# Optimization experiments

Hardware: AMD Instinct MI355X
Metric: run time of the kernel (lower is better)

Reference implementation:

```python
import jax, jax.numpy as jnp
import numpy as np

# static config (matches init_kwargs / input_specs)
LENS = (2048, 1024, 512, 256)   # per-level temporal lengths, sum = 3840
N, LQ, D_MODEL = 8, 2048, 256
M, L, P = 8, 4, 4               # heads, levels, points
D_HEAD = D_MODEL // M           # 32


def setup_inputs() -> dict:
    key = jax.random.key(0)
    ks = jax.random.split(key, 8)
    s = 0.02  # xavier-ish scale for 256-wide linears
    return {
        "query": jax.random.normal(ks[0], (N, LQ, D_MODEL), jnp.float32),
        "reference_points": jax.random.uniform(ks[1], (N, LQ, L, 1), dtype=jnp.float32),
        "input_flatten": jax.random.normal(ks[2], (N, sum(LENS), D_MODEL), jnp.float32),
        "input_temporal_lens": jnp.array(LENS, jnp.int32),
        "input_level_start_index": jnp.array(np.concatenate([[0], np.cumsum(LENS)[:-1]]), jnp.int32),
        "W_val": jax.random.normal(ks[3], (D_MODEL, D_MODEL), jnp.float32) * s,
        "b_val": jnp.zeros((D_MODEL,), jnp.float32),
        "W_off": jax.random.normal(ks[4], (M * L * P, D_MODEL), jnp.float32) * s,
        "b_off": jax.random.normal(ks[5], (M * L * P,), jnp.float32),  # mimics linspace bias init
        "W_attn": jax.random.normal(ks[6], (M * L * P, D_MODEL), jnp.float32) * s,
        "b_attn": jnp.zeros((M * L * P,), jnp.float32),
    }


def _sample_level(v, x, T):
    """1D bilinear sampling with zero padding, matching F.grid_sample
    (mode='bilinear', padding_mode='zeros', align_corners=False) on a (1,T) map.
    v: (N, T, M, D) level values; x: (N, Lq, M, P) normalized locations in [0,1].
    Returns (N, Lq, M, P, D)."""
    n, lq, m, p = x.shape
    ix = x * T - 0.5
    ix0 = jnp.floor(ix)
    w1 = (ix - ix0)[..., None]            # (N,Lq,M,P,1)
    i0 = ix0.astype(jnp.int32)

    def gather(idx):
        valid = ((idx >= 0) & (idx < T)).astype(v.dtype)
        idxc = jnp.clip(idx, 0, T - 1)
        flat = idxc.transpose(0, 1, 3, 2).reshape(n, lq * p, m)       # (N, Lq*P, M)
        g = jnp.take_along_axis(v, flat[..., None], axis=1)           # (N, Lq*P, M, D)
        g = g * valid.transpose(0, 1, 3, 2).reshape(n, lq * p, m)[..., None]
        return g.reshape(n, lq, p, m, -1).transpose(0, 1, 3, 2, 4)    # (N,Lq,M,P,D)

    return gather(i0) * (1.0 - w1) + gather(i0 + 1) * w1


def _deform_core(value, lens, loc, attn):
    """value: (N, S, M, D); loc: (N,Lq,M,L,P,1); attn: (N,Lq,M,L,P) -> (N,Lq,M*D)"""
    out = 0.0
    start = 0
    for lid, T in enumerate(lens):
        v = value[:, start:start + T]
        start += T
        s = _sample_level(v, loc[:, :, :, lid, :, 0], T)              # (N,Lq,M,P,D)
        out = out + jnp.einsum('nqmpd,nqmp->nqmd', s, attn[:, :, :, lid])
    n, lq, m, d = out.shape
    return out.reshape(n, lq, m * d)


def reference(query, reference_points, input_flatten, input_temporal_lens,
              input_level_start_index, W_val, b_val, W_off, b_off, W_attn, b_attn):
    lens = LENS  # static per-level lengths (needed for static slicing)
    value = (input_flatten @ W_val.T + b_val).reshape(N, sum(lens), M, D_HEAD)
    offs = (query @ W_off.T + b_off).reshape(N, LQ, M, L, P, 1)
    attn = jax.nn.softmax((query @ W_attn.T + b_attn).reshape(N, LQ, M, L * P), axis=-1)
    attn = attn.reshape(N, LQ, M, L, P)
    # reference_points last dim == 1, offset_normalizer=None branch
    norm = jnp.asarray(lens, query.dtype)[None, None, None, :, None, None]
    loc = reference_points[:, :, None, :, None, :] + offs / norm      # (N,Lq,M,L,P,1)
    # fp32 path of the torch module returns the core output WITHOUT output_proj
    return _deform_core(value, lens, loc, attn)
```

## Files before the change

kernel.cpp:

```cpp
#include <hip/hip_runtime.h>
#include <cstddef>

namespace {

constexpr int NB    = 8;
constexpr int LQn   = 2048;
constexpr int DM    = 256;
constexpr int S_TOT = 3840;

typedef __attribute__((ext_vector_type(8))) short  short8;
typedef __attribute__((ext_vector_type(4))) float  f32x4;
typedef __attribute__((ext_vector_type(8))) _Float16 half8;
typedef __attribute__((ext_vector_type(4))) _Float16 half4;
typedef __attribute__((ext_vector_type(2))) _Float16 half2v;

__device__ inline unsigned short f2bf(float f) {
  union { float f; unsigned u; } v; v.f = f;
  const unsigned u = v.u;
  return (unsigned short)((u + 0x7FFFu + ((u >> 16) & 1u)) >> 16);
}

__global__ __launch_bounds__(256) void gemm_bf16_k(
    const float* __restrict__ A_val, const float* __restrict__ A_prj,
    const float* __restrict__ W_val, const float* __restrict__ b_val,
    const float* __restrict__ W_off, const float* __restrict__ b_off,
    const float* __restrict__ W_att, const float* __restrict__ b_att,
    _Float16* __restrict__ out_val, _Float16* __restrict__ out_prj)
{
  __shared__ short As[128 * 64];
  __shared__ short Bs[128 * 64];

  const int tid  = threadIdx.x;
  const int lane = tid & 63;
  const int wid  = tid >> 6;
  const int wm   = wid >> 1;
  const int wn   = wid & 1;

  const int id = blockIdx.x;
  const float *A, *W, *bias;
  _Float16* out;
  int r0, c0;
  if (id < 480) {
    const int rb = id >> 1, c = id & 1;
    A = A_val; out = out_val; r0 = rb * 128; c0 = c * 128;
    W = W_val + (size_t)c0 * DM; bias = b_val + c0;
  } else {
    const int j = id - 480, rb = j >> 1, c = j & 1;
    A = A_prj; out = out_prj; r0 = rb * 128; c0 = c * 128;
    W = c ? W_att : W_off; bias = c ? b_att : b_off;
  }

  f32x4 acc[4][4] = {};

  float bv[4];
  #pragma unroll
  for (int ni = 0; ni < 4; ++ni)
    bv[ni] = bias[wn * 64 + ni * 16 + (lane & 15)];

  f32x4 pa0[4], pa1[4], pw0[4], pw1[4];

  auto load_tiles = [&](int k0) {
    #pragma unroll
    for (int i = 0; i < 4; ++i) {
      const int ch  = tid + i * 256;
      const int row = ch >> 3;
      const int kg  = ch & 7;
      const size_t goff = (size_t)(r0 + row) * DM + k0 + kg * 8;
      pa0[i] = *reinterpret_cast<const f32x4*>(&A[goff]);
      pa1[i] = *reinterpret_cast<const f32x4*>(&A[goff + 4]);
      const size_t woff = (size_t)row * DM + k0 + kg * 8;
      pw0[i] = *reinterpret_cast<const f32x4*>(&W[woff]);
      pw1[i] = *reinterpret_cast<const f32x4*>(&W[woff + 4]);
    }
  };

  load_tiles(0);

  for (int k = 0; k < 4; ++k) {
    #pragma unroll
    for (int i = 0; i < 4; ++i) {
      const int ch  = tid + i * 256;
      const int row = ch >> 3;
      const int kg  = ch & 7;
      short8 sa, sw;
      #pragma unroll
      for (int j = 0; j < 4; ++j) {
        sa[j]     = (short)f2bf(pa0[i][j]);
        sa[j + 4] = (short)f2bf(pa1[i][j]);
        sw[j]     = (short)f2bf(pw0[i][j]);
        sw[j + 4] = (short)f2bf(pw1[i][j]);
      }
      const int byte = row * 128 + ((kg * 16) ^ ((row & 7) << 4));
      *reinterpret_cast<short8*>(reinterpret_cast<char*>(As) + byte) = sa;
      *reinterpret_cast<short8*>(reinterpret_cast<char*>(Bs) + byte) = sw;
    }
    if (k < 3) load_tiles((k + 1) * 64);

    asm volatile("s_waitcnt lgkmcnt(0)" ::: "memory");
    __builtin_amdgcn_sched_barrier(0);
    __builtin_amdgcn_s_barrier();
    __builtin_amdgcn_sched_barrier(0);

    #pragma unroll
    for (int ks = 0; ks < 2; ++ks) {
      const int kb = (ks * 32 + (lane >> 4) * 8) * 2;
      short8 af[4], bf[4];
      #pragma unroll
      for (int mi = 0; mi < 4; ++mi) {
        const int row = wm * 64 + mi * 16 + (lane & 15);
        const int byte = row * 128 + (kb ^ ((row & 7) << 4));
        af[mi] = *reinterpret_cast<const short8*>(
            reinterpret_cast<const char*>(As) + byte);
      }
      #pragma unroll
      for (int ni = 0; ni < 4; ++ni) {
        const int col = wn * 64 + ni * 16 + (lane & 15);
        const int byte = col * 128 + (kb ^ ((col & 7) << 4));
        bf[ni] = *reinterpret_cast<const short8*>(
            reinterpret_cast<const char*>(Bs) + byte);
      }
      #pragma unroll
      for (int mi = 0; mi < 4; ++mi)
        #pragma unroll
        for (int ni = 0; ni < 4; ++ni)
          acc[mi][ni] = __builtin_amdgcn_mfma_f32_16x16x32_bf16(
              af[mi], bf[ni], acc[mi][ni], 0, 0, 0);
    }

    asm volatile("s_waitcnt lgkmcnt(0)" ::: "memory");
    __builtin_amdgcn_sched_barrier(0);
    __builtin_amdgcn_s_barrier();
    __builtin_amdgcn_sched_barrier(0);
  }

  #pragma unroll
  for (int mi = 0; mi < 4; ++mi) {
    const int row = r0 + wm * 64 + mi * 16 + (lane >> 4) * 4;
    #pragma unroll
    for (int ni = 0; ni < 4; ++ni) {
      const int col = c0 + wn * 64 + ni * 16 + (lane & 15);
      #pragma unroll
      for (int j = 0; j < 4; ++j)
        out[(size_t)(row + j) * DM + col] = (_Float16)(acc[mi][ni][j] + bv[ni]);
    }
  }
}

__global__ __launch_bounds__(512) void sample_k(
    const _Float16* __restrict__ proj,
    const float* __restrict__ refp,
    const _Float16* __restrict__ value,
    float* __restrict__ out)
{
  __shared__ uint4 tap_s[8][136];

  const int d     = blockIdx.x;
  const int n     = d & 7;
  const int chunk = d >> 3;
  const int row0q = n * LQn + chunk * 8;
  const int t     = threadIdx.x;

  const int lens[4]   = {2048, 1024, 512, 256};
  const int starts[4] = {0, 2048, 3072, 3584};

  if (t < 256) {
    const int q   = t >> 5;
    const int m   = (t >> 2) & 7;
    const int sub = t & 3;
    const int j0  = m * 16 + sub * 4;
    const size_t prow = (size_t)(row0q + q) * DM;

    const half4 offv = *reinterpret_cast<const half4*>(&proj[prow + j0]);
    const half4 lgv  = *reinterpret_cast<const half4*>(&proj[prow + 128 + j0]);
    float lg[4], off[4];
    #pragma unroll
    for (int i = 0; i < 4; ++i) { lg[i] = (float)lgv[i]; off[i] = (float)offv[i]; }

    float mx = fmaxf(fmaxf(lg[0], lg[1]), fmaxf(lg[2], lg[3]));
    mx = fmaxf(mx, __shfl_xor(mx, 1));
    mx = fmaxf(mx, __shfl_xor(mx, 2));
    float e[4], s = 0.f;
    #pragma unroll
    for (int i = 0; i < 4; ++i) { e[i] = __expf(lg[i] - mx); s += e[i]; }
    s += __shfl_xor(s, 1);
    s += __shfl_xor(s, 2);
    const float inv = 1.f / s;

    const int   T  = lens[sub];
    const int   st = starts[sub];
    const float fT = (float)T;
    const float rf = refp[(size_t)(row0q + q) * 4 + sub];
    #pragma unroll
    for (int i = 0; i < 4; ++i) {
      const float a  = e[i] * inv;
      const float ix = fmaf(rf, fT, off[i] - 0.5f);
      const float fl = floorf(ix);
      const float w1 = ix - fl;
      const int   i0 = (int)fl;
      const int   i1 = i0 + 1;
      const float wa = (i0 >= 0 && i0 < T) ? a * (1.f - w1) : 0.f;
      const float wb = (i1 >= 0 && i1 < T) ? a * w1 : 0.f;
      const int   r0b = (st + min(max(i0, 0), T - 1)) * 512;
      const int   r1b = (st + min(max(i1, 0), T - 1)) * 512;
      union { half2v h; unsigned u; } pw;
      pw.h.x = (_Float16)wa; pw.h.y = (_Float16)wb;
      uint4 ent; ent.x = pw.u; ent.y = (unsigned)r0b; ent.z = (unsigned)r1b; ent.w = 0u;
      tap_s[q][m * 17 + sub * 4 + i] = ent;
    }
  }
  __syncthreads();

  const int q  = t >> 6;
  const int l  = t & 63;
  const int m  = l >> 3;
  const int dg = l & 3;
  const int th = (l >> 2) & 1;
  const char* vb = reinterpret_cast<const char*>(value) +
                   (size_t)n * S_TOT * 512 + m * 64 + dg * 16;

  float acc[8] = {};
  #pragma unroll
  for (int i = 0; i < 8; ++i) {
    const uint4 e = tap_s[q][m * 17 + th * 8 + i];
    union { unsigned u; half2v h; } pw; pw.u = e.x;
    const float wa = (float)pw.h.x;
    const float wb = (float)pw.h.y;
    const half8 v0 = *reinterpret_cast<const half8*>(vb + e.y);
    const half8 v1 = *reinterpret_cast<const half8*>(vb + e.z);
    #pragma unroll
    for (int j = 0; j < 8; ++j)
      acc[j] = fmaf(wa, (float)v0[j], fmaf(wb, (float)v1[j], acc[j]));
  }

  #pragma unroll
  for (int j = 0; j < 8; ++j) acc[j] += __shfl_xor(acc[j], 4);

  if (th == 0) {
    float* op = &out[(size_t)(row0q + q) * DM + m * 32 + dg * 8];
    f32x4 o0 = {acc[0], acc[1], acc[2], acc[3]};
    f32x4 o1 = {acc[4], acc[5], acc[6], acc[7]};
    *reinterpret_cast<f32x4*>(op)     = o0;
    *reinterpret_cast<f32x4*>(op + 4) = o1;
  }
}

}

extern "C" void kernel_launch(void* const* d_in, const int* in_sizes, int n_in,
                              void* d_out, int out_size, void* d_ws, size_t ws_size,
                              hipStream_t stream) {
  const float* query  = (const float*)d_in[0];
  const float* refp   = (const float*)d_in[1];
  const float* inflat = (const float*)d_in[2];
  const float* W_val  = (const float*)d_in[5];
  const float* b_val  = (const float*)d_in[6];
  const float* W_off  = (const float*)d_in[7];
  const float* b_off  = (const float*)d_in[8];
  const float* W_attn = (const float*)d_in[9];
  const float* b_attn = (const float*)d_in[10];
  float* out = (float*)d_out;

  _Float16* value_h = (_Float16*)d_ws;
  _Float16* proj_h  = (_Float16*)((char*)d_ws +
                      (size_t)NB * S_TOT * DM * sizeof(_Float16));

  gemm_bf16_k<<<dim3(736), dim3(256), 0, stream>>>(
      inflat, query, W_val, b_val, W_off, b_off, W_attn, b_attn,
      value_h, proj_h);

  sample_k<<<dim3(NB * LQn / 8), dim3(512), 0, stream>>>(
      proj_h, refp, value_h, out);
}
```

Before: 43.93 us.

## Pre-convert weights to swizzled bf16 blob and stream via global_load_lds

A small kernel now converts the three weight matrices once per call into a pre-swizzled bf16 blob. The GEMM then loads each B tile straight into LDS with global_load_lds, which drops the per-block fp32 weight loads, the bf16 conversion and the LDS stores. This cuts register pressure and weight bandwidth in the main GEMM, at the cost of an extra kernel launch and a finer vmcnt wait that is sensitive to the order of outstanding loads.

```diff
diff --git a/kernel.cpp b/kernel.cpp
--- a/kernel.cpp
+++ b/kernel.cpp
@@ -20,11 +20,45 @@
   return (unsigned short)((u + 0x7FFFu + ((u >> 16) & 1u)) >> 16);
 }
 
+__device__ inline void load_lds16(const void* g, void* l) {
+  __builtin_amdgcn_global_load_lds(
+      (const __attribute__((address_space(1))) void*)g,
+      (__attribute__((address_space(3))) void*)l, 16, 0, 0);
+}
+
+__global__ __launch_bounds__(256) void wconv_k(
+    const float* __restrict__ W_val, const float* __restrict__ W_off,
+    const float* __restrict__ W_att, unsigned short* __restrict__ blob)
+{
+  const int g     = blockIdx.x * 256 + threadIdx.x;
+  const int tile  = g >> 10;
+  const int ch    = g & 1023;
+  const int which = tile >> 2;
+  const int kt    = tile & 3;
+  const int row   = ch >> 3;
+  const int kg    = (ch & 7) ^ (row & 7);
+  const float* src;
+  if (which == 0)      src = W_val + (size_t)row * DM;
+  else if (which == 1) src = W_val + (size_t)(128 + row) * DM;
+  else if (which == 2) src = W_off + (size_t)row * DM;
+  else                 src = W_att + (size_t)row * DM;
+  const int col = kt * 64 + kg * 8;
+  const f32x4 w0 = *reinterpret_cast<const f32x4*>(&src[col]);
+  const f32x4 w1 = *reinterpret_cast<const f32x4*>(&src[col + 4]);
+  short8 s;
+  #pragma unroll
+  for (int j = 0; j < 4; ++j) {
+    s[j]     = (short)f2bf(w0[j]);
+    s[j + 4] = (short)f2bf(w1[j]);
+  }
+  *reinterpret_cast<short8*>(&blob[(size_t)g * 8]) = s;
+}
+
 __global__ __launch_bounds__(256) void gemm_bf16_k(
     const float* __restrict__ A_val, const float* __restrict__ A_prj,
-    const float* __restrict__ W_val, const float* __restrict__ b_val,
-    const float* __restrict__ W_off, const float* __restrict__ b_off,
-    const float* __restrict__ W_att, const float* __restrict__ b_att,
+    const unsigned short* __restrict__ wblob,
+    const float* __restrict__ b_val,
+    const float* __restrict__ b_off, const float* __restrict__ b_att,
     _Float16* __restrict__ out_val, _Float16* __restrict__ out_prj)
 {
   __shared__ short As[128 * 64];
@@ -37,18 +71,21 @@
   const int wn   = wid & 1;
 
   const int id = blockIdx.x;
-  const float *A, *W, *bias;
+  const float* A;
+  const float* bias;
   _Float16* out;
-  int r0, c0;
+  int r0, c0, which;
   if (id < 480) {
     const int rb = id >> 1, c = id & 1;
     A = A_val; out = out_val; r0 = rb * 128; c0 = c * 128;
-    W = W_val + (size_t)c0 * DM; bias = b_val + c0;
+    which = c; bias = b_val + c * 128;
   } else {
     const int j = id - 480, rb = j >> 1, c = j & 1;
     A = A_prj; out = out_prj; r0 = rb * 128; c0 = c * 128;
-    W = c ? W_att : W_off; bias = c ? b_att : b_off;
-  }
+    which = 2 + c; bias = c ? b_att : b_off;
+  }
+  const char* wbase = reinterpret_cast<const char*>(wblob) +
+                      (size_t)which * 4 * 16384;
 
   f32x4 acc[4][4] = {};
 
@@ -57,9 +94,9 @@
   for (int ni = 0; ni < 4; ++ni)
     bv[ni] = bias[wn * 64 + ni * 16 + (lane & 15)];
 
-  f32x4 pa0[4], pa1[4], pw0[4], pw1[4];
-
-  auto load_tiles = [&](int k0) {
+  f32x4 pa0[4], pa1[4];
+
+  auto load_A = [&](int k0) {
     #pragma unroll
     for (int i = 0; i < 4; ++i) {
       const int ch  = tid + i * 256;
@@ -68,35 +105,40 @@
       const size_t goff = (size_t)(r0 + row) * DM + k0 + kg * 8;
       pa0[i] = *reinterpret_cast<const f32x4*>(&A[goff]);
       pa1[i] = *reinterpret_cast<const f32x4*>(&A[goff + 4]);
-      const size_t woff = (size_t)row * DM + k0 + kg * 8;
-      pw0[i] = *reinterpret_cast<const f32x4*>(&W[woff]);
-      pw1[i] = *reinterpret_cast<const f32x4*>(&W[woff + 4]);
     }
   };
 
-  load_tiles(0);
-
+  load_A(0);
+
+  #pragma unroll
   for (int k = 0; k < 4; ++k) {
+    {
+      const char* wsrc = wbase + (size_t)k * 16384;
+      #pragma unroll
+      for (int i = 0; i < 4; ++i) {
+        const int off = (tid + i * 256) * 16;
+        load_lds16(wsrc + off, reinterpret_cast<char*>(Bs) + off);
+      }
+    }
+    __builtin_amdgcn_sched_barrier(0);
+
     #pragma unroll
     for (int i = 0; i < 4; ++i) {
       const int ch  = tid + i * 256;
       const int row = ch >> 3;
       const int kg  = ch & 7;
-      short8 sa, sw;
+      short8 sa;
       #pragma unroll
       for (int j = 0; j < 4; ++j) {
         sa[j]     = (short)f2bf(pa0[i][j]);
         sa[j + 4] = (short)f2bf(pa1[i][j]);
-        sw[j]     = (short)f2bf(pw0[i][j]);
-        sw[j + 4] = (short)f2bf(pw1[i][j]);
       }
       const int byte = row * 128 + ((kg * 16) ^ ((row & 7) << 4));
       *reinterpret_cast<short8*>(reinterpret_cast<char*>(As) + byte) = sa;
-      *reinterpret_cast<short8*>(reinterpret_cast<char*>(Bs) + byte) = sw;
-    }
-    if (k < 3) load_tiles((k + 1) * 64);
-
-    asm volatile("s_waitcnt lgkmcnt(0)" ::: "memory");
+    }
+    load_A(k < 3 ? (k + 1) * 64 : 0);
+
+    asm volatile("s_waitcnt vmcnt(8) lgkmcnt(0)" ::: "memory");
     __builtin_amdgcn_sched_barrier(0);
     __builtin_amdgcn_s_barrier();
     __builtin_amdgcn_sched_barrier(0);
@@ -261,12 +303,13 @@
   float* out = (float*)d_out;
 
   _Float16* value_h = (_Float16*)d_ws;
-  _Float16* proj_h  = (_Float16*)((char*)d_ws +
-                      (size_t)NB * S_TOT * DM * sizeof(_Float16));
+  _Float16* proj_h  = (_Float16*)((char*)d_ws + (size_t)15728640);
+  unsigned short* wblob = (unsigned short*)((char*)d_ws + (size_t)24117248);
+
+  wconv_k<<<dim3(64), dim3(256), 0, stream>>>(W_val, W_off, W_attn, wblob);
 
   gemm_bf16_k<<<dim3(736), dim3(256), 0, stream>>>(
-      inflat, query, W_val, b_val, W_off, b_off, W_attn, b_attn,
-      value_h, proj_h);
+      inflat, query, wblob, b_val, b_off, b_attn, value_h, proj_h);
 
   sample_k<<<dim3(NB * LQn / 8), dim3(512), 0, stream>>>(
       proj_h, refp, value_h, out);
```

New measurement: 48.47 us. 1.1x slower.
